# Optimization experiments

Measured on AMD Instinct MI355X. Metric: run time of the kernel, lower is better.

The kernel has to match this reference:

```python
import jax, jax.numpy as jnp
import numpy as np

N_NODES = 10000
N_EDGES = 160000
N_GRAPHS = 16
IN_FEAT = 128
DIMS = [(128, 512), (512, 256), (256, 64), (64, 32)]


def _lin_params(key, fin, fout):
    w = jax.random.normal(key, (fin, fout), jnp.float32) * (1.0 / np.sqrt(fin))
    b = jnp.zeros((fout,), jnp.float32)
    return w, b


def setup_inputs() -> dict:
    key = jax.random.key(0)
    ks = jax.random.split(key, 64)
    inp = {}
    inp['x'] = jax.random.normal(ks[0], (N_NODES, IN_FEAT), jnp.float32)
    inp['edge_index'] = jax.random.randint(ks[1], (2, N_EDGES), 0, N_NODES, jnp.int64 if jax.config.jax_enable_x64 else jnp.int32)
    inp['batch'] = jnp.sort(jax.random.randint(ks[2], (N_NODES,), 0, N_GRAPHS))
    ki = 3
    for li, (fin, fout) in enumerate(DIMS, start=1):
        for nm in ['q', 'k', 'v', 's']:
            w, b = _lin_params(ks[ki], fin, fout); ki += 1
            inp[f'W{nm}{li}'] = w
            inp[f'b{nm}{li}'] = b
    inp['Wg'], inp['bg'] = _lin_params(ks[ki], 32, 1); ki += 1
    inp['Wf'], inp['bf'] = _lin_params(ks[ki], 32, 9)
    return inp


def _segment_softmax(logits, seg, num_segments):
    m = jax.ops.segment_max(logits, seg, num_segments=num_segments)
    e = jnp.exp(logits - m[seg])
    s = jax.ops.segment_sum(e, seg, num_segments=num_segments)
    return e / s[seg]


def _transformer_conv(x, src, dst, Wq, bq, Wk, bk, Wv, bv, Ws, bs):
    # PyG TransformerConv, heads=1: attention over incoming edges per dst node.
    n = x.shape[0]
    q = x @ Wq + bq
    k = x @ Wk + bk
    v = x @ Wv + bv
    d = q.shape[-1]
    logits = jnp.sum(q[dst] * k[src], axis=-1) / jnp.sqrt(jnp.asarray(d, x.dtype))
    alpha = _segment_softmax(logits, dst, n)  # [E]
    agg = jax.ops.segment_sum(alpha[:, None] * v[src], dst, num_segments=n)
    return agg + (x @ Ws + bs)  # root/skip connection


def reference(x, edge_index, batch,
              Wq1, bq1, Wk1, bk1, Wv1, bv1, Ws1, bs1,
              Wq2, bq2, Wk2, bk2, Wv2, bv2, Ws2, bs2,
              Wq3, bq3, Wk3, bk3, Wv3, bv3, Ws3, bs3,
              Wq4, bq4, Wk4, bk4, Wv4, bv4, Ws4, bs4,
              Wg, bg, Wf, bf):
    src, dst = edge_index[0], edge_index[1]
    layers = [
        (Wq1, bq1, Wk1, bk1, Wv1, bv1, Ws1, bs1),
        (Wq2, bq2, Wk2, bk2, Wv2, bv2, Ws2, bs2),
        (Wq3, bq3, Wk3, bk3, Wv3, bv3, Ws3, bs3),
        (Wq4, bq4, Wk4, bk4, Wv4, bv4, Ws4, bs4),
    ]
    h = x
    for p in layers:
        h = jax.nn.elu(_transformer_conv(h, src, dst, *p))
    # GlobalAttention pooling: gate softmax per graph, weighted sum.
    gate = (h @ Wg + bg)[:, 0]  # [N]
    a = _segment_softmax(gate, batch, N_GRAPHS)
    pooled = jax.ops.segment_sum(a[:, None] * h, batch, num_segments=N_GRAPHS)  # [G, 32]
    return pooled @ Wf + bf  # [G, 9]
```

## Files before the change

### kernel.cpp

```cpp
#include <hip/hip_runtime.h>
#include <hip/hip_bf16.h>
#include <math.h>


typedef __bf16 bf16x8 __attribute__((ext_vector_type(8)));
typedef __bf16 bf16x4 __attribute__((ext_vector_type(4)));
typedef __bf16 bf16x2 __attribute__((ext_vector_type(2)));
typedef float f32x4 __attribute__((ext_vector_type(4)));
typedef float f32x2 __attribute__((ext_vector_type(2)));

#define GBM 128
#define GBN 128
#define GBK 64

#if __has_builtin(__builtin_amdgcn_global_load_lds)
#define ASYNC_LDS 1
__device__ __forceinline__ void gload16(const __bf16* g, __bf16* l) {
  __builtin_amdgcn_global_load_lds(
      (const __attribute__((address_space(1))) unsigned int*)g,
      (__attribute__((address_space(3))) unsigned int*)l, 16, 0, 0);
}
#endif

#if __has_builtin(__builtin_amdgcn_fdot2_f32_bf16)
#define HAS_BF16_DOT2 1
#endif

__global__ __launch_bounds__(256) void gemm_mfma_kernel(
    const __bf16* __restrict__ A, const __bf16* __restrict__ Bt,
    const float* __restrict__ bias, __bf16* __restrict__ qkvs,
    int M, int K, int Nc) {
  __shared__ __bf16 As[GBM * 64];
  __shared__ __bf16 Bs[GBN * 64];
  const int tid = threadIdx.x;
  const int wave = tid >> 6;
  const int lane = tid & 63;
  const int quad = lane >> 4;
  const int l16 = lane & 15;
  const int m0 = blockIdx.y * GBM;
  const int n0 = blockIdx.x * GBN;
  const int wm = (wave & 1) * 64;
  const int wn = (wave >> 1) * 64;

  const int r8 = lane >> 3;
  const int sseg = lane & 7;

  f32x4 acc[4][4] = {};

  for (int k0 = 0; k0 < K; k0 += GBK) {
#pragma unroll
    for (int it = 0; it < 4; ++it) {
      const int rbase = wave * 32 + it * 8;
      const int row = rbase + r8;
      const int sw = sseg ^ r8;
      const __bf16* ga = A + (size_t)(m0 + row) * K + k0 + sw * 8;
      const __bf16* gb = Bt + (size_t)(n0 + row) * K + k0 + sw * 8;
#ifdef ASYNC_LDS
      gload16(ga, As + rbase * 64);
      gload16(gb, Bs + rbase * 64);
#else
      *(bf16x8*)(As + row * 64 + sseg * 8) = *(const bf16x8*)ga;
      *(bf16x8*)(Bs + row * 64 + sseg * 8) = *(const bf16x8*)gb;
#endif
    }
    __syncthreads();

#pragma unroll
    for (int ks = 0; ks < 2; ++ks) {
      bf16x8 af[4], bfr[4];
#pragma unroll
      for (int i = 0; i < 4; ++i) {
        const int ra = wm + i * 16 + l16;
        const int rb = wn + i * 16 + l16;
        const int ps = ((ks * 4 + quad) ^ (l16 & 7)) * 8;
        af[i]  = *(const bf16x8*)(As + ra * 64 + ps);
        bfr[i] = *(const bf16x8*)(Bs + rb * 64 + ps);
      }
#pragma unroll
      for (int mi = 0; mi < 4; ++mi)
#pragma unroll
        for (int ni = 0; ni < 4; ++ni)
          acc[mi][ni] = __builtin_amdgcn_mfma_f32_16x16x32_bf16(
              af[mi], bfr[ni], acc[mi][ni], 0, 0, 0);
    }
    __syncthreads();
  }

  float bsv[4];
#pragma unroll
  for (int ni = 0; ni < 4; ++ni) bsv[ni] = bias[n0 + wn + ni * 16 + l16];
#pragma unroll
  for (int mi = 0; mi < 4; ++mi) {
#pragma unroll
    for (int r = 0; r < 4; ++r) {
      int row = m0 + wm + mi * 16 + quad * 4 + r;
      if (row < M) {
        size_t rb = (size_t)row * Nc;
#pragma unroll
        for (int ni = 0; ni < 4; ++ni) {
          int col = n0 + wn + ni * 16 + l16;
          qkvs[rb + col] = (__bf16)(acc[mi][ni][r] + bsv[ni]);
        }
      }
    }
  }
}

#define WTOT 860160
#define BTOT 3456
#define XTOT 320000
__global__ void pack_all_kernel(
    const float* W0q, const float* W0k, const float* W0v, const float* W0s,
    const float* b0q, const float* b0k, const float* b0v, const float* b0s,
    const float* W1q, const float* W1k, const float* W1v, const float* W1s,
    const float* b1q, const float* b1k, const float* b1v, const float* b1s,
    const float* W2q, const float* W2k, const float* W2v, const float* W2s,
    const float* b2q, const float* b2k, const float* b2v, const float* b2s,
    const float* W3q, const float* W3k, const float* W3v, const float* W3s,
    const float* b3q, const float* b3k, const float* b3v, const float* b3s,
    const float* __restrict__ x, __bf16* __restrict__ xb,
    __bf16* __restrict__ Wt, float* __restrict__ bcat,
    const int* __restrict__ dst, int* __restrict__ deg, int E) {
  const int t = blockIdx.x * 256 + threadIdx.x;
  if (t < WTOT) {
    int l, local, ksh, fsh;
    if (t < 262144)      { l = 0; local = t;          ksh = 7; fsh = 9; }
    else if (t < 786432) { l = 1; local = t - 262144; ksh = 9; fsh = 8; }
    else if (t < 851968) { l = 2; local = t - 786432; ksh = 8; fsh = 6; }
    else                 { l = 3; local = t - 851968; ksh = 6; fsh = 5; }
    const int K = 1 << ksh, fout = 1 << fsh;
    int c = local >> ksh;
    int kk = local & (K - 1);
    int blk = c >> fsh;
    int j = c & (fout - 1);
    const float* W;
    if (l == 0)      W = blk == 0 ? W0q : blk == 1 ? W0k : blk == 2 ? W0v : W0s;
    else if (l == 1) W = blk == 0 ? W1q : blk == 1 ? W1k : blk == 2 ? W1v : W1s;
    else if (l == 2) W = blk == 0 ? W2q : blk == 1 ? W2k : blk == 2 ? W2v : W2s;
    else             W = blk == 0 ? W3q : blk == 1 ? W3k : blk == 2 ? W3v : W3s;
    Wt[t] = (__bf16)W[((size_t)kk << fsh) + j];
  } else if (t < WTOT + BTOT) {
    int u = t - WTOT;
    int l, local, fsh, boff;
    if (u < 2048)      { l = 0; local = u;        fsh = 9; boff = 0; }
    else if (u < 3072) { l = 1; local = u - 2048; fsh = 8; boff = 2048; }
    else if (u < 3328) { l = 2; local = u - 3072; fsh = 6; boff = 3072; }
    else               { l = 3; local = u - 3328; fsh = 5; boff = 3328; }
    const int fout = 1 << fsh;
    int blk = local >> fsh, j = local & (fout - 1);
    const float* b;
    if (l == 0)      b = blk == 0 ? b0q : blk == 1 ? b0k : blk == 2 ? b0v : b0s;
    else if (l == 1) b = blk == 0 ? b1q : blk == 1 ? b1k : blk == 2 ? b1v : b1s;
    else if (l == 2) b = blk == 0 ? b2q : blk == 1 ? b2k : blk == 2 ? b2v : b2s;
    else             b = blk == 0 ? b3q : blk == 1 ? b3k : blk == 2 ? b3v : b3s;
    bcat[boff + local] = b[j];
  } else if (t < WTOT + BTOT + XTOT) {
    int i = t - (WTOT + BTOT);
    float4 v = ((const float4*)x)[i];
    bf16x4 o;
    o[0] = (__bf16)v.x; o[1] = (__bf16)v.y; o[2] = (__bf16)v.z; o[3] = (__bf16)v.w;
    *(bf16x4*)(xb + (size_t)i * 4) = o;
  } else if (t < WTOT + BTOT + XTOT + E) {
    int e = t - (WTOT + BTOT + XTOT);
    atomicAdd(&deg[dst[e]], 1);
  }
}

__global__ __launch_bounds__(1024) void scan_kernel(const int* __restrict__ deg,
                                                    int* __restrict__ offs, int N) {
  __shared__ int sums[1024];
  const int tid = threadIdx.x;
  const int chunk = (N + 1023) / 1024;
  const int start = tid * chunk;
  int s = 0;
  for (int i = 0; i < chunk; ++i) {
    int idx = start + i;
    if (idx < N) s += deg[idx];
  }
  sums[tid] = s;
  __syncthreads();
  for (int off = 1; off < 1024; off <<= 1) {
    int t = (tid >= off) ? sums[tid - off] : 0;
    __syncthreads();
    sums[tid] += t;
    __syncthreads();
  }
  int run = (tid == 0) ? 0 : sums[tid - 1];
  for (int i = 0; i < chunk; ++i) {
    int idx = start + i;
    if (idx < N) {
      offs[idx] = run;
      run += deg[idx];
    }
  }
  if (tid == 1023) offs[N] = sums[1023];
}

__global__ void scatter_kernel(const int* __restrict__ src, const int* __restrict__ dst,
                               const int* __restrict__ offs, int* __restrict__ cursor,
                               int* __restrict__ csr_src, int E) {
  int e = blockIdx.x * blockDim.x + threadIdx.x;
  if (e >= E) return;
  int d = dst[e];
  int pos = offs[d] + atomicAdd(&cursor[d], 1);
  csr_src[pos] = src[e];
}

template <int D, int LPG_LOG2, bool GATE>
__global__ __launch_bounds__(256) void attn_fused_kernel(
    const __bf16* __restrict__ qkvs, const int* __restrict__ csr_src,
    const int* __restrict__ offs, __bf16* __restrict__ h_out, int N,
    float scale, const float* __restrict__ Wg, const float* __restrict__ bg,
    float* __restrict__ gate_out) {
  constexpr int LPG = 1 << LPG_LOG2;
  constexpr int NG = 64 / LPG;
  constexpr int NIT = D / (8 * LPG);
  constexpr int LD = 4 * D;
  const int node = (blockIdx.x * 256 + threadIdx.x) >> 6;
  const int lane = threadIdx.x & 63;
  if (node >= N) return;
  const int g = lane >> LPG_LOG2;
  const int l = lane & (LPG - 1);
  const int begin = offs[node];
  const int deg = offs[node + 1] - begin;

  const __bf16* qrow = qkvs + (size_t)node * LD;
  bf16x8 qreg[NIT];
#pragma unroll
  for (int it = 0; it < NIT; ++it)
    qreg[it] = *(const bf16x8*)(qrow + it * LPG * 8 + l * 8);

  float m0 = 0.f;
  float s = 0.f;
  f32x2 acc[NIT][4] = {};

  for (int base = 0; base < deg; base += NG) {
    const int i = base + g;
    const bool valid = i < deg;
    const int sidx = valid ? csr_src[begin + i] : 0;
    const __bf16* krow = qkvs + (size_t)sidx * LD + D;
    bf16x8 kv[NIT], vv[NIT];
    if (valid) {
#pragma unroll
      for (int it = 0; it < NIT; ++it) {
        kv[it] = *(const bf16x8*)(krow + it * LPG * 8 + l * 8);
        vv[it] = *(const bf16x8*)(krow + D + it * LPG * 8 + l * 8);
      }
    }
    float p = 0.f;
    if (valid) {
#ifdef HAS_BF16_DOT2
#pragma unroll
      for (int it = 0; it < NIT; ++it)
#pragma unroll
        for (int j2 = 0; j2 < 4; ++j2) {
          bf16x2 qa; qa[0] = qreg[it][2 * j2]; qa[1] = qreg[it][2 * j2 + 1];
          bf16x2 ka; ka[0] = kv[it][2 * j2];   ka[1] = kv[it][2 * j2 + 1];
          p = __builtin_amdgcn_fdot2_f32_bf16(qa, ka, p, false);
        }
#else
#pragma unroll
      for (int it = 0; it < NIT; ++it)
#pragma unroll
        for (int j = 0; j < 8; ++j) p += (float)qreg[it][j] * (float)kv[it][j];
#endif
    }
#pragma unroll
    for (int off = LPG >> 1; off; off >>= 1) p += __shfl_xor(p, off);
    const float logit = valid ? p * scale : -INFINITY;

    if (base == 0) {
      float mm = logit;
#pragma unroll
      for (int off = LPG; off < 64; off <<= 1)
        mm = fmaxf(mm, __shfl_xor(mm, off));
      m0 = mm;
    }

    const float w = __expf(logit - m0);
    s += w;
    if (valid) {
      f32x2 w2; w2[0] = w; w2[1] = w;
#pragma unroll
      for (int it = 0; it < NIT; ++it)
#pragma unroll
        for (int j2 = 0; j2 < 4; ++j2) {
          f32x2 vf;
          vf[0] = (float)vv[it][2 * j2];
          vf[1] = (float)vv[it][2 * j2 + 1];
          acc[it][j2] += w2 * vf;
        }
    }
  }

#pragma unroll
  for (int off = LPG; off < 64; off <<= 1) {
    s += __shfl_xor(s, off);
#pragma unroll
    for (int it = 0; it < NIT; ++it)
#pragma unroll
      for (int j2 = 0; j2 < 4; ++j2) {
        acc[it][j2][0] += __shfl_xor(acc[it][j2][0], off);
        acc[it][j2][1] += __shfl_xor(acc[it][j2][1], off);
      }
  }
  const float inv = (deg > 0) ? (1.0f / s) : 0.f;

  if (g == 0) {
    float rr[NIT][8];
#pragma unroll
    for (int it = 0; it < NIT; ++it) {
      const int f0 = it * LPG * 8 + l * 8;
      bf16x8 sk = *(const bf16x8*)(qrow + 3 * D + f0);
      bf16x8 o;
#pragma unroll
      for (int j2 = 0; j2 < 4; ++j2) {
        float r0 = acc[it][j2][0] * inv + (float)sk[2 * j2];
        float r1 = acc[it][j2][1] * inv + (float)sk[2 * j2 + 1];
        r0 = (r0 > 0.f) ? r0 : expm1f(r0);
        r1 = (r1 > 0.f) ? r1 : expm1f(r1);
        rr[it][2 * j2] = r0;
        rr[it][2 * j2 + 1] = r1;
        o[2 * j2] = (__bf16)r0;
        o[2 * j2 + 1] = (__bf16)r1;
      }
      *(bf16x8*)(h_out + (size_t)node * D + f0) = o;
    }
    if (GATE) {
      float gp = 0.f;
#pragma unroll
      for (int j = 0; j < 8; ++j) gp += rr[0][j] * Wg[l * 8 + j];
#pragma unroll
      for (int off = 1; off < LPG; off <<= 1) gp += __shfl_xor(gp, off);
      if (l == 0) gate_out[node] = gp + bg[0];
    }
  }
}

__global__ __launch_bounds__(256) void pool_final_kernel(
    const __bf16* __restrict__ h, const float* __restrict__ gate,
    const int* __restrict__ batch, int N, const float* __restrict__ Wf,
    const float* __restrict__ bf_, float* __restrict__ out) {
  __shared__ float red[256];
  __shared__ float pooled_s[32];
  __shared__ float m_s, inv_s;
  __shared__ int sb[2];
  const int g = blockIdx.x;
  const int tid = threadIdx.x;

  if (tid < 2) {
    int target = g + tid;
    int lo = 0, hi = N;
    while (lo < hi) {
      int mid = (lo + hi) >> 1;
      if (batch[mid] < target) lo = mid + 1;
      else hi = mid;
    }
    sb[tid] = lo;
  }
  __syncthreads();
  const int s = sb[0];
  const int e_end = sb[1];

  float m = -INFINITY;
  for (int i = s + tid; i < e_end; i += 256) m = fmaxf(m, gate[i]);
  red[tid] = m;
  __syncthreads();
  for (int off = 128; off; off >>= 1) {
    if (tid < off) red[tid] = fmaxf(red[tid], red[tid + off]);
    __syncthreads();
  }
  if (tid == 0) m_s = red[0];
  __syncthreads();
  m = m_s;

  float ss = 0.f;
  for (int i = s + tid; i < e_end; i += 256) ss += __expf(gate[i] - m);
  red[tid] = ss;
  __syncthreads();
  for (int off = 128; off; off >>= 1) {
    if (tid < off) red[tid] += red[tid + off];
    __syncthreads();
  }
  if (tid == 0) inv_s = (e_end > s) ? (1.0f / red[0]) : 0.f;
  __syncthreads();
  const float inv = inv_s;

  const int f = tid & 31;
  const int grp = tid >> 5;
  float acc = 0.f;
  for (int i = s + grp; i < e_end; i += 8)
    acc += __expf(gate[i] - m) * (float)h[(size_t)i * 32 + f];
  red[tid] = acc;
  __syncthreads();
  if (tid < 32) {
    float a = 0.f;
#pragma unroll
    for (int j = 0; j < 8; ++j) a += red[j * 32 + tid];
    pooled_s[tid] = a * inv;
  }
  __syncthreads();

  if (tid < 9) {
    float o = bf_[tid];
#pragma unroll
    for (int kk = 0; kk < 32; ++kk) o += pooled_s[kk] * Wf[kk * 9 + tid];
    out[g * 9 + tid] = o;
  }
}

extern "C" void kernel_launch(void* const* d_in, const int* in_sizes, int n_in,
                              void* d_out, int out_size, void* d_ws, size_t ws_size,
                              hipStream_t stream) {
  const int N = in_sizes[2];
  const int E = in_sizes[1] / 2;
  const int G = 16;
  const int NP = N + 128;

  const float* x = (const float*)d_in[0];
  const int* ei = (const int*)d_in[1];
  const int* batch = (const int*)d_in[2];
  const int* src = ei;
  const int* dst = ei + E;
  const float* Wg = (const float*)d_in[35];
  const float* bg = (const float*)d_in[36];
  const float* Wf = (const float*)d_in[37];
  const float* bf_ = (const float*)d_in[38];
  float* out = (float*)d_out;

  char* p = (char*)d_ws;
  auto carve = [&](size_t bytes) -> char* {
    char* r = p;
    p += (bytes + 255) & ~(size_t)255;
    return r;
  };
  int* deg = (int*)carve((size_t)2 * N * 4);
  int* cursor = deg + N;
  int* offs = (int*)carve((size_t)(N + 1) * 4);
  int* csr_src = (int*)carve((size_t)E * 4);
  __bf16* Ab = (__bf16*)carve((size_t)NP * 128 * 2);
  __bf16* Wt = (__bf16*)carve((size_t)WTOT * 2);
  float* bcat = (float*)carve(BTOT * 4);
  __bf16* qkvs = (__bf16*)carve((size_t)N * 2048 * 2);
  __bf16* ha = (__bf16*)carve((size_t)NP * 512 * 2);
  __bf16* hb = (__bf16*)carve((size_t)NP * 512 * 2);
  float* gate = (float*)carve((size_t)N * 4);
  (void)ws_size;

  hipMemsetAsync(deg, 0, (size_t)2 * N * 4, stream);
  const float** di = (const float**)d_in;
  pack_all_kernel<<<(WTOT + BTOT + XTOT + E + 255) / 256, 256, 0, stream>>>(
      di[3], di[5], di[7], di[9], di[4], di[6], di[8], di[10],
      di[11], di[13], di[15], di[17], di[12], di[14], di[16], di[18],
      di[19], di[21], di[23], di[25], di[20], di[22], di[24], di[26],
      di[27], di[29], di[31], di[33], di[28], di[30], di[32], di[34],
      x, Ab, Wt, bcat, dst, deg, E);
  scan_kernel<<<1, 1024, 0, stream>>>(deg, offs, N);
  scatter_kernel<<<(E + 255) / 256, 256, 0, stream>>>(src, dst, offs, cursor, csr_src, E);

  const int fins[4] = {128, 512, 256, 64};
  const int fouts[4] = {512, 256, 64, 32};
  const size_t woffs[4] = {0, 262144, 786432, 851968};
  const int boffs[4] = {0, 2048, 3072, 3328};
  const __bf16* hin = Ab;
  __bf16* houts[4] = {ha, hb, ha, hb};
  const int agrid = ((size_t)N * 64 + 255) / 256;

  for (int l = 0; l < 4; ++l) {
    const int fin = fins[l], fout = fouts[l];
    const int Nc = 4 * fout;
    __bf16* hout = houts[l];

    dim3 grid(Nc / GBN, (N + GBM - 1) / GBM);
    gemm_mfma_kernel<<<grid, 256, 0, stream>>>(hin, Wt + woffs[l], bcat + boffs[l],
                                               qkvs, N, fin, Nc);

    float scale = 1.0f / sqrtf((float)fout);
    if (l == 0) {
      attn_fused_kernel<512, 4, false><<<agrid, 256, 0, stream>>>(
          qkvs, csr_src, offs, hout, N, scale, nullptr, nullptr, nullptr);
    } else if (l == 1) {
      attn_fused_kernel<256, 4, false><<<agrid, 256, 0, stream>>>(
          qkvs, csr_src, offs, hout, N, scale, nullptr, nullptr, nullptr);
    } else if (l == 2) {
      attn_fused_kernel<64, 3, false><<<agrid, 256, 0, stream>>>(
          qkvs, csr_src, offs, hout, N, scale, nullptr, nullptr, nullptr);
    } else {
      attn_fused_kernel<32, 2, true><<<agrid, 256, 0, stream>>>(
          qkvs, csr_src, offs, hout, N, scale, Wg, bg, gate);
    }
    hin = hout;
  }

  pool_final_kernel<<<G, 256, 0, stream>>>(hin, gate, batch, N, Wf, bf_, out);
}
```

Measured before the change: 344.8 us.

## Reassociate first transformer layer to attend in 128-dim input space

Layer 1 is restructured algebraically. Query and key projections fold into one precomputed 128x128 matrix (Wq·Wkᵀ) plus a bias term, so logits become u_dst·x_src over 128 features. Values are aggregated in the 128-dim input space and then projected once, together with the skip path, by a fused GEMM whose epilogue adds biases and applies ELU. This avoids computing and gathering 512-wide q/k/v per edge. In exchange it adds weight-product precompute in the pack kernel, and the rounding order changes, including dropping the q-bias/k constant term, which softmax cancels.

Measured after the change: 341.6 us. About the same (-0.9%).

```diff
diff --git a/kernel.cpp b/kernel.cpp
--- a/kernel.cpp
+++ b/kernel.cpp
@@ -106,9 +106,100 @@
   }
 }
 
+__global__ __launch_bounds__(256) void gemm_mfma_elu_kernel(
+    const __bf16* __restrict__ A, const __bf16* __restrict__ Bt,
+    const float* __restrict__ bias_s, const float* __restrict__ bias_v,
+    const int* __restrict__ offs, __bf16* __restrict__ out,
+    int M, int K, int Nc) {
+  __shared__ __bf16 As[GBM * 64];
+  __shared__ __bf16 Bs[GBN * 64];
+  const int tid = threadIdx.x;
+  const int wave = tid >> 6;
+  const int lane = tid & 63;
+  const int quad = lane >> 4;
+  const int l16 = lane & 15;
+  const int m0 = blockIdx.y * GBM;
+  const int n0 = blockIdx.x * GBN;
+  const int wm = (wave & 1) * 64;
+  const int wn = (wave >> 1) * 64;
+
+  const int r8 = lane >> 3;
+  const int sseg = lane & 7;
+
+  f32x4 acc[4][4] = {};
+
+  for (int k0 = 0; k0 < K; k0 += GBK) {
+#pragma unroll
+    for (int it = 0; it < 4; ++it) {
+      const int rbase = wave * 32 + it * 8;
+      const int row = rbase + r8;
+      const int sw = sseg ^ r8;
+      const __bf16* ga = A + (size_t)(m0 + row) * K + k0 + sw * 8;
+      const __bf16* gb = Bt + (size_t)(n0 + row) * K + k0 + sw * 8;
+#ifdef ASYNC_LDS
+      gload16(ga, As + rbase * 64);
+      gload16(gb, Bs + rbase * 64);
+#else
+      *(bf16x8*)(As + row * 64 + sseg * 8) = *(const bf16x8*)ga;
+      *(bf16x8*)(Bs + row * 64 + sseg * 8) = *(const bf16x8*)gb;
+#endif
+    }
+    __syncthreads();
+
+#pragma unroll
+    for (int ks = 0; ks < 2; ++ks) {
+      bf16x8 af[4], bfr[4];
+#pragma unroll
+      for (int i = 0; i < 4; ++i) {
+        const int ra = wm + i * 16 + l16;
+        const int rb = wn + i * 16 + l16;
+        const int ps = ((ks * 4 + quad) ^ (l16 & 7)) * 8;
+        af[i]  = *(const bf16x8*)(As + ra * 64 + ps);
+        bfr[i] = *(const bf16x8*)(Bs + rb * 64 + ps);
+      }
+#pragma unroll
+      for (int mi = 0; mi < 4; ++mi)
+#pragma unroll
+        for (int ni = 0; ni < 4; ++ni)
+          acc[mi][ni] = __builtin_amdgcn_mfma_f32_16x16x32_bf16(
+              af[mi], bfr[ni], acc[mi][ni], 0, 0, 0);
+    }
+    __syncthreads();
+  }
+
+  float bsv[4], bvv[4];
+#pragma unroll
+  for (int ni = 0; ni < 4; ++ni) {
+    const int col = n0 + wn + ni * 16 + l16;
+    bsv[ni] = bias_s[col];
+    bvv[ni] = bias_v[col];
+  }
+#pragma unroll
+  for (int mi = 0; mi < 4; ++mi) {
+#pragma unroll
+    for (int r = 0; r < 4; ++r) {
+      int row = m0 + wm + mi * 16 + quad * 4 + r;
+      if (row < M) {
+        const float bm = (offs[row + 1] - offs[row]) > 0 ? 1.f : 0.f;
+        size_t rb = (size_t)row * Nc;
+#pragma unroll
+        for (int ni = 0; ni < 4; ++ni) {
+          int col = n0 + wn + ni * 16 + l16;
+          float v = acc[mi][ni][r] + bsv[ni] + bm * bvv[ni];
+          v = (v > 0.f) ? v : expm1f(v);
+          out[rb + col] = (__bf16)v;
+        }
+      }
+    }
+  }
+}
+
 #define WTOT 860160
 #define BTOT 3456
 #define XTOT 320000
+#define ATOT 16384
+#define UBTOT 128
+#define B2TOT 131072
 __global__ void pack_all_kernel(
     const float* W0q, const float* W0k, const float* W0v, const float* W0s,
     const float* b0q, const float* b0k, const float* b0v, const float* b0s,
@@ -120,7 +211,9 @@
     const float* b3q, const float* b3k, const float* b3v, const float* b3s,
     const float* __restrict__ x, __bf16* __restrict__ xb,
     __bf16* __restrict__ Wt, float* __restrict__ bcat,
-    const int* __restrict__ dst, int* __restrict__ deg, int E) {
+    const int* __restrict__ dst, int* __restrict__ deg, int E,
+    __bf16* __restrict__ Abt, float* __restrict__ biasu,
+    __bf16* __restrict__ Bt2) {
   const int t = blockIdx.x * 256 + threadIdx.x;
   if (t < WTOT) {
     int l, local, ksh, fsh;
@@ -163,6 +256,39 @@
   } else if (t < WTOT + BTOT + XTOT + E) {
     int e = t - (WTOT + BTOT + XTOT);
     atomicAdd(&deg[dst[e]], 1);
+  } else {
+    int u2 = t - (WTOT + BTOT + XTOT + E);
+    if (u2 < ATOT) {
+      const int n = u2 >> 7;
+      const int k = u2 & 127;
+      const float4* wq = (const float4*)(W0q + (size_t)k * 512);
+      const float4* wk = (const float4*)(W0k + (size_t)n * 512);
+      float sacc = 0.f;
+#pragma unroll 4
+      for (int j = 0; j < 128; ++j) {
+        float4 a = wq[j], b = wk[j];
+        sacc += a.x * b.x + a.y * b.y + a.z * b.z + a.w * b.w;
+      }
+      Abt[(size_t)n * 128 + k] = (__bf16)sacc;
+    } else if (u2 < ATOT + UBTOT) {
+      const int n = u2 - ATOT;
+      const float4* wk = (const float4*)(W0k + (size_t)n * 512);
+      const float4* bq = (const float4*)b0q;
+      float sacc = 0.f;
+#pragma unroll 4
+      for (int j = 0; j < 128; ++j) {
+        float4 a = wk[j], b = bq[j];
+        sacc += a.x * b.x + a.y * b.y + a.z * b.z + a.w * b.w;
+      }
+      biasu[n] = sacc;
+    } else if (u2 < ATOT + UBTOT + B2TOT) {
+      const int i = u2 - (ATOT + UBTOT);
+      const int n = i >> 8;
+      const int k = i & 255;
+      float v = (k < 128) ? W0v[(size_t)k * 512 + n]
+                          : W0s[(size_t)(k - 128) * 512 + n];
+      Bt2[(size_t)n * 256 + k] = (__bf16)v;
+    }
   }
 }
 
@@ -337,6 +463,120 @@
   }
 }
 
+template <int LPG_LOG2>
+__global__ __launch_bounds__(256) void attn_lin_kernel(
+    const __bf16* __restrict__ u, const __bf16* __restrict__ hsrc,
+    const int* __restrict__ csr_src, const int* __restrict__ offs,
+    __bf16* __restrict__ buf, int N, float scale) {
+  constexpr int D = 128;
+  constexpr int LPG = 1 << LPG_LOG2;
+  constexpr int NG = 64 / LPG;
+  constexpr int NIT = D / (8 * LPG);
+  const int node = (blockIdx.x * 256 + threadIdx.x) >> 6;
+  const int lane = threadIdx.x & 63;
+  if (node >= N) return;
+  const int g = lane >> LPG_LOG2;
+  const int l = lane & (LPG - 1);
+  const int begin = offs[node];
+  const int deg = offs[node + 1] - begin;
+
+  const __bf16* urow = u + (size_t)node * D;
+  bf16x8 qreg[NIT];
+#pragma unroll
+  for (int it = 0; it < NIT; ++it)
+    qreg[it] = *(const bf16x8*)(urow + it * LPG * 8 + l * 8);
+
+  float m0 = 0.f;
+  float s = 0.f;
+  f32x2 acc[NIT][4] = {};
+
+  for (int base = 0; base < deg; base += NG) {
+    const int i = base + g;
+    const bool valid = i < deg;
+    const int sidx = valid ? csr_src[begin + i] : 0;
+    const __bf16* hr = hsrc + (size_t)sidx * D;
+    bf16x8 kv[NIT];
+    if (valid) {
+#pragma unroll
+      for (int it = 0; it < NIT; ++it)
+        kv[it] = *(const bf16x8*)(hr + it * LPG * 8 + l * 8);
+    }
+    float p = 0.f;
+    if (valid) {
+#ifdef HAS_BF16_DOT2
+#pragma unroll
+      for (int it = 0; it < NIT; ++it)
+#pragma unroll
+        for (int j2 = 0; j2 < 4; ++j2) {
+          bf16x2 qa; qa[0] = qreg[it][2 * j2]; qa[1] = qreg[it][2 * j2 + 1];
+          bf16x2 ka; ka[0] = kv[it][2 * j2];   ka[1] = kv[it][2 * j2 + 1];
+          p = __builtin_amdgcn_fdot2_f32_bf16(qa, ka, p, false);
+        }
+#else
+#pragma unroll
+      for (int it = 0; it < NIT; ++it)
+#pragma unroll
+        for (int j = 0; j < 8; ++j) p += (float)qreg[it][j] * (float)kv[it][j];
+#endif
+    }
+#pragma unroll
+    for (int off = LPG >> 1; off; off >>= 1) p += __shfl_xor(p, off);
+    const float logit = valid ? p * scale : -INFINITY;
+
+    if (base == 0) {
+      float mm = logit;
+#pragma unroll
+      for (int off = LPG; off < 64; off <<= 1)
+        mm = fmaxf(mm, __shfl_xor(mm, off));
+      m0 = mm;
+    }
+
+    const float w = __expf(logit - m0);
+    s += w;
+    if (valid) {
+      f32x2 w2; w2[0] = w; w2[1] = w;
+#pragma unroll
+      for (int it = 0; it < NIT; ++it)
+#pragma unroll
+        for (int j2 = 0; j2 < 4; ++j2) {
+          f32x2 vf;
+          vf[0] = (float)kv[it][2 * j2];
+          vf[1] = (float)kv[it][2 * j2 + 1];
+          acc[it][j2] += w2 * vf;
+        }
+    }
+  }
+
+#pragma unroll
+  for (int off = LPG; off < 64; off <<= 1) {
+    s += __shfl_xor(s, off);
+#pragma unroll
+    for (int it = 0; it < NIT; ++it)
+#pragma unroll
+      for (int j2 = 0; j2 < 4; ++j2) {
+        acc[it][j2][0] += __shfl_xor(acc[it][j2][0], off);
+        acc[it][j2][1] += __shfl_xor(acc[it][j2][1], off);
+      }
+  }
+  const float inv = (deg > 0) ? (1.0f / s) : 0.f;
+
+  if (g == 0) {
+#pragma unroll
+    for (int it = 0; it < NIT; ++it) {
+      const int f0 = it * LPG * 8 + l * 8;
+      bf16x8 o;
+#pragma unroll
+      for (int j2 = 0; j2 < 4; ++j2) {
+        o[2 * j2]     = (__bf16)(acc[it][j2][0] * inv);
+        o[2 * j2 + 1] = (__bf16)(acc[it][j2][1] * inv);
+      }
+      *(bf16x8*)(buf + (size_t)node * 256 + f0) = o;
+      *(bf16x8*)(buf + (size_t)node * 256 + 128 + f0) =
+          *(const bf16x8*)(hsrc + (size_t)node * D + f0);
+    }
+  }
+}
+
 __global__ __launch_bounds__(256) void pool_final_kernel(
     const __bf16* __restrict__ h, const float* __restrict__ gate,
     const int* __restrict__ batch, int N, const float* __restrict__ Wf,
@@ -441,48 +681,63 @@
   __bf16* Ab = (__bf16*)carve((size_t)NP * 128 * 2);
   __bf16* Wt = (__bf16*)carve((size_t)WTOT * 2);
   float* bcat = (float*)carve(BTOT * 4);
-  __bf16* qkvs = (__bf16*)carve((size_t)N * 2048 * 2);
+  __bf16* qkvs = (__bf16*)carve((size_t)NP * 1024 * 2);
   __bf16* ha = (__bf16*)carve((size_t)NP * 512 * 2);
   __bf16* hb = (__bf16*)carve((size_t)NP * 512 * 2);
   float* gate = (float*)carve((size_t)N * 4);
+  __bf16* ubuf = (__bf16*)carve((size_t)NP * 128 * 2);
+  __bf16* cat = (__bf16*)carve((size_t)NP * 256 * 2);
+  __bf16* Abt = (__bf16*)carve((size_t)ATOT * 2);
+  float* biasu = (float*)carve((size_t)UBTOT * 4);
+  __bf16* Bt2 = (__bf16*)carve((size_t)B2TOT * 2);
   (void)ws_size;
 
   hipMemsetAsync(deg, 0, (size_t)2 * N * 4, stream);
   const float** di = (const float**)d_in;
-  pack_all_kernel<<<(WTOT + BTOT + XTOT + E + 255) / 256, 256, 0, stream>>>(
+  pack_all_kernel<<<(WTOT + BTOT + XTOT + E + ATOT + UBTOT + B2TOT + 255) / 256,
+                    256, 0, stream>>>(
       di[3], di[5], di[7], di[9], di[4], di[6], di[8], di[10],
       di[11], di[13], di[15], di[17], di[12], di[14], di[16], di[18],
       di[19], di[21], di[23], di[25], di[20], di[22], di[24], di[26],
       di[27], di[29], di[31], di[33], di[28], di[30], di[32], di[34],
-      x, Ab, Wt, bcat, dst, deg, E);
+      x, Ab, Wt, bcat, dst, deg, E, Abt, biasu, Bt2);
   scan_kernel<<<1, 1024, 0, stream>>>(deg, offs, N);
   scatter_kernel<<<(E + 255) / 256, 256, 0, stream>>>(src, dst, offs, cursor, csr_src, E);
 
-  const int fins[4] = {128, 512, 256, 64};
-  const int fouts[4] = {512, 256, 64, 32};
-  const size_t woffs[4] = {0, 262144, 786432, 851968};
-  const int boffs[4] = {0, 2048, 3072, 3328};
-  const __bf16* hin = Ab;
-  __bf16* houts[4] = {ha, hb, ha, hb};
   const int agrid = ((size_t)N * 64 + 255) / 256;
-
-  for (int l = 0; l < 4; ++l) {
+  const int mg = (N + GBM - 1) / GBM;
+
+  {
+    dim3 g1(1, mg);
+    gemm_mfma_kernel<<<g1, 256, 0, stream>>>(Ab, Abt, biasu, ubuf, N, 128, 128);
+    attn_lin_kernel<3><<<agrid, 256, 0, stream>>>(ubuf, Ab, csr_src, offs, cat, N,
+                                                  1.0f / sqrtf(512.f));
+    dim3 g2(4, mg);
+    gemm_mfma_elu_kernel<<<g2, 256, 0, stream>>>(cat, Bt2, di[10], di[8], offs,
+                                                 ha, N, 256, 512);
+  }
+
+  const int fins[3] = {512, 256, 64};
+  const int fouts[3] = {256, 64, 32};
+  const size_t woffs[3] = {262144, 786432, 851968};
+  const int boffs[3] = {2048, 3072, 3328};
+  const __bf16* hin = ha;
+  __bf16* houts[3] = {hb, ha, hb};
+
+  for (int l = 0; l < 3; ++l) {
     const int fin = fins[l], fout = fouts[l];
     const int Nc = 4 * fout;
     __bf16* hout = houts[l];
 
-    dim3 grid(Nc / GBN, (N + GBM - 1) / GBM);
+    dim3 grid(Nc / GBN, mg);
     gemm_mfma_kernel<<<grid, 256, 0, stream>>>(hin, Wt + woffs[l], bcat + boffs[l],
                                                qkvs, N, fin, Nc);
 
     float scale = 1.0f / sqrtf((float)fout);
     if (l == 0) {
-      attn_fused_kernel<512, 4, false><<<agrid, 256, 0, stream>>>(
+      attn_fused_kernel<256, 4, false><<<agrid, 256, 0, stream>>>(
           qkvs, csr_src, offs, hout, N, scale, nullptr, nullptr, nullptr);
     } else if (l == 1) {
-      attn_fused_kernel<256, 4, false><<<agrid, 256, 0, stream>>>(
-          qkvs, csr_src, offs, hout, N, scale, nullptr, nullptr, nullptr);
-    } else if (l == 2) {
       attn_fused_kernel<64, 3, false><<<agrid, 256, 0, stream>>>(
           qkvs, csr_src, offs, hout, N, scale, nullptr, nullptr, nullptr);
     } else {
```
